# Optimization experiments

Measured on AMD Instinct MI355X. Metric: run time of the kernel, lower is better.

The kernel has to match this reference:

```python
import jax, jax.numpy as jnp
import numpy as np

EMBED = 512
HEADS = 8
HEAD_DIM = EMBED // HEADS
MLP_HIDDEN = EMBED * 4
EPS = 1e-5


def _layernorm(x, g, b):
    mu = jnp.mean(x, axis=-1, keepdims=True)
    var = jnp.var(x, axis=-1, keepdims=True)
    return (x - mu) * jax.lax.rsqrt(var + EPS) * g + b


def setup_inputs() -> dict:
    key = jax.random.key(0)
    ks = jax.random.split(key, 12)
    s = 0.02
    return {
        "x": jax.random.normal(ks[0], (4, 2048, EMBED), dtype=jnp.float32),
        "ln1_g": jnp.ones((EMBED,), jnp.float32),
        "ln1_b": jnp.zeros((EMBED,), jnp.float32),
        "w_qkv": jax.random.normal(ks[1], (EMBED, 3 * EMBED), jnp.float32) * s,
        "b_qkv": jnp.zeros((3 * EMBED,), jnp.float32),
        "w_proj": jax.random.normal(ks[2], (EMBED, EMBED), jnp.float32) * s,
        "b_proj": jnp.zeros((EMBED,), jnp.float32),
        "ln2_g": jnp.ones((EMBED,), jnp.float32),
        "ln2_b": jnp.zeros((EMBED,), jnp.float32),
        "w1": jax.random.normal(ks[3], (EMBED, MLP_HIDDEN), jnp.float32) * s,
        "b1": jnp.zeros((MLP_HIDDEN,), jnp.float32),
        "w2": jax.random.normal(ks[4], (MLP_HIDDEN, EMBED), jnp.float32) * s,
        "b2": jnp.zeros((EMBED,), jnp.float32),
    }


def reference(x, ln1_g, ln1_b, w_qkv, b_qkv, w_proj, b_proj, ln2_g, ln2_b, w1, b1, w2, b2):
    B, N, C = x.shape
    scale = HEAD_DIM ** -0.5
    h = _layernorm(x, ln1_g, ln1_b)
    qkv = h @ w_qkv + b_qkv                       # [B,N,3C]
    qkv = qkv.reshape(B, N, 3, HEADS, HEAD_DIM)
    q = qkv[:, :, 0].transpose(0, 2, 1, 3)        # [B,H,N,D]
    k = qkv[:, :, 1].transpose(0, 2, 1, 3)
    v = qkv[:, :, 2].transpose(0, 2, 1, 3)
    attn = jnp.einsum('bhnd,bhmd->bhnm', q, k) * scale
    attn = jax.nn.softmax(attn, axis=-1)
    h = jnp.einsum('bhnm,bhmd->bhnd', attn, v)    # [B,H,N,D]
    h = h.transpose(0, 2, 1, 3).reshape(B, N, C)
    h = h @ w_proj + b_proj
    x = x + h
    m = _layernorm(x, ln2_g, ln2_b)
    m = jax.nn.gelu(m @ w1 + b1, approximate=False) @ w2 + b2
    return x + m
```

## Files before the change

kernel.cpp:

```cpp
#include <hip/hip_runtime.h>
#include <hip/hip_bf16.h>

typedef unsigned short u16;
typedef unsigned int u32;
typedef __attribute__((ext_vector_type(8))) __bf16 bf16x8;
typedef __attribute__((ext_vector_type(4))) float f32x4;
typedef __attribute__((ext_vector_type(16))) float f32x16;

#define LOG2E 1.4426950408889634f

__device__ __forceinline__ u16 f2bf(float f) {
  union { __hip_bfloat16 h; u16 u; } cv;
  cv.h = __float2bfloat16(f);
  return cv.u;
}

__device__ __forceinline__ float bf2f(u16 u) {
  union { u32 u; float f; } cv;
  cv.u = ((u32)u) << 16;
  return cv.f;
}

__device__ __forceinline__ u32 pk2(float a, float b) {
  return (u32)f2bf(a) | ((u32)f2bf(b) << 16);
}

#define EXP2 __builtin_amdgcn_exp2f

__device__ __forceinline__ f32x4 mfma16(bf16x8 a, bf16x8 b, f32x4 c) {
  return __builtin_amdgcn_mfma_f32_16x16x32_bf16(a, b, c, 0, 0, 0);
}
__device__ __forceinline__ f32x16 mfma32(bf16x8 a, bf16x8 b, f32x16 c) {
  return __builtin_amdgcn_mfma_f32_32x32x16_bf16(a, b, c, 0, 0, 0);
}

__device__ __forceinline__ void gload16(const u16* g, u16* lds) {
  __builtin_amdgcn_global_load_lds(
      (const __attribute__((address_space(1))) u32*)g,
      (__attribute__((address_space(3))) u32*)lds, 16, 0, 0);
}

__global__ __launch_bounds__(256) void prep_kernel(
    const float* __restrict__ w_qkv, u16* __restrict__ wqkvT,
    const float* __restrict__ w_proj, u16* __restrict__ wprojT,
    const float* __restrict__ w1, u16* __restrict__ w1T,
    const float* __restrict__ w2, u16* __restrict__ w2T,
    const float* __restrict__ X, const float* __restrict__ gam,
    const float* __restrict__ bet, u16* __restrict__ Y) {
  __shared__ float T[64][65];
  const int bid = blockIdx.x;
  if (bid < 768) {
    const float* W; u16* WT; int K, N, base;
    if (bid < 192)      { W = w_qkv; WT = wqkvT; K = 512;  N = 1536; base = 0; }
    else if (bid < 256) { W = w_proj; WT = wprojT; K = 512; N = 512; base = 192; }
    else if (bid < 512) { W = w1;   WT = w1T;   K = 512;  N = 2048; base = 256; }
    else                { W = w2;   WT = w2T;   K = 2048; N = 512;  base = 512; }
    int b = bid - base;
    int ntx = N >> 6;
    int bx = b % ntx, by = b / ntx;
    int tx = threadIdx.x & 63, ty = threadIdx.x >> 6;
#pragma unroll
    for (int i = 0; i < 64; i += 4)
      T[ty + i][tx] = W[(size_t)(by * 64 + ty + i) * N + bx * 64 + tx];
    __syncthreads();
#pragma unroll
    for (int i = 0; i < 64; i += 4)
      WT[(size_t)(bx * 64 + ty + i) * K + by * 64 + tx] = f2bf(T[tx][ty + i]);
  } else {
    int wid = threadIdx.x >> 6, l = threadIdx.x & 63;
    int row = (bid - 768) * 4 + wid;
    const float4* xp = reinterpret_cast<const float4*>(X + (size_t)row * 512);
    float4 a = xp[l], c = xp[l + 64];
    float s  = a.x + a.y + a.z + a.w + c.x + c.y + c.z + c.w;
    float s2 = a.x*a.x + a.y*a.y + a.z*a.z + a.w*a.w
             + c.x*c.x + c.y*c.y + c.z*c.z + c.w*c.w;
#pragma unroll
    for (int m = 1; m < 64; m <<= 1) { s += __shfl_xor(s, m); s2 += __shfl_xor(s2, m); }
    float mu = s * (1.f / 512.f);
    float rs = rsqrtf(s2 * (1.f / 512.f) - mu * mu + 1e-5f);
    const float4* gp = reinterpret_cast<const float4*>(gam);
    const float4* bp = reinterpret_cast<const float4*>(bet);
    float4 g0 = gp[l], g1 = gp[l + 64], b0 = bp[l], b1 = bp[l + 64];
    ushort4 o;
    o.x = f2bf((a.x - mu) * rs * g0.x + b0.x);
    o.y = f2bf((a.y - mu) * rs * g0.y + b0.y);
    o.z = f2bf((a.z - mu) * rs * g0.z + b0.z);
    o.w = f2bf((a.w - mu) * rs * g0.w + b0.w);
    reinterpret_cast<ushort4*>(Y + (size_t)row * 512)[l] = o;
    o.x = f2bf((c.x - mu) * rs * g1.x + b1.x);
    o.y = f2bf((c.y - mu) * rs * g1.y + b1.y);
    o.z = f2bf((c.z - mu) * rs * g1.z + b1.z);
    o.w = f2bf((c.w - mu) * rs * g1.w + b1.w);
    reinterpret_cast<ushort4*>(Y + (size_t)row * 512)[l + 64] = o;
  }
}

__global__ __launch_bounds__(64) void ln_kernel(const float* __restrict__ X,
                                                const float* __restrict__ gam,
                                                const float* __restrict__ bet,
                                                u16* __restrict__ Y) {
  int row = blockIdx.x, l = threadIdx.x;
  const float4* xp = reinterpret_cast<const float4*>(X + (size_t)row * 512);
  float4 a = xp[l], c = xp[l + 64];
  float s  = a.x + a.y + a.z + a.w + c.x + c.y + c.z + c.w;
  float s2 = a.x*a.x + a.y*a.y + a.z*a.z + a.w*a.w
           + c.x*c.x + c.y*c.y + c.z*c.z + c.w*c.w;
#pragma unroll
  for (int m = 1; m < 64; m <<= 1) { s += __shfl_xor(s, m); s2 += __shfl_xor(s2, m); }
  float mu = s * (1.f / 512.f);
  float rs = rsqrtf(s2 * (1.f / 512.f) - mu * mu + 1e-5f);
  const float4* gp = reinterpret_cast<const float4*>(gam);
  const float4* bp = reinterpret_cast<const float4*>(bet);
  float4 g0 = gp[l], g1 = gp[l + 64], b0 = bp[l], b1 = bp[l + 64];
  ushort4 o;
  o.x = f2bf((a.x - mu) * rs * g0.x + b0.x);
  o.y = f2bf((a.y - mu) * rs * g0.y + b0.y);
  o.z = f2bf((a.z - mu) * rs * g0.z + b0.z);
  o.w = f2bf((a.w - mu) * rs * g0.w + b0.w);
  reinterpret_cast<ushort4*>(Y + (size_t)row * 512)[l] = o;
  o.x = f2bf((c.x - mu) * rs * g1.x + b1.x);
  o.y = f2bf((c.y - mu) * rs * g1.y + b1.y);
  o.z = f2bf((c.z - mu) * rs * g1.z + b1.z);
  o.w = f2bf((c.w - mu) * rs * g1.w + b1.w);
  reinterpret_cast<ushort4*>(Y + (size_t)row * 512)[l + 64] = o;
}

template <int EPI, int BM>
__global__ __launch_bounds__(256) void gemm_bt(
    const u16* __restrict__ A, const u16* __restrict__ BT,
    int M, int N, int K,
    const float* __restrict__ bias,
    const float* __restrict__ resid,
    float* __restrict__ outF,
    u16* __restrict__ outU,
    u16* __restrict__ Qo, u16* __restrict__ Ko, u16* __restrict__ VTo) {
  constexpr int MFR = BM / 32;
  constexpr int CA = BM / 64;
  __shared__ u16 As[2][BM * 32];
  __shared__ u16 Bs[2][128 * 32];
  const int tid = threadIdx.x;
  const int wid = tid >> 6, l = tid & 63;
  const int lg = l >> 4, ll = l & 15;
  const int nx = gridDim.x;
  const int id = blockIdx.y * nx + blockIdx.x;
  const int cpx = (nx * gridDim.y) >> 3;
  const int wg = (id & 7) * cpx + (id >> 3);
  const int m0 = (wg / nx) * BM, n0 = (wg % nx) * 128;
  const int wm = (wid >> 1) * (BM / 2), wn = (wid & 1) * 64;
  const f32x4 zf = {0.f, 0.f, 0.f, 0.f};
  f32x4 acc[MFR][4];
#pragma unroll
  for (int i = 0; i < MFR; i++)
#pragma unroll
    for (int j = 0; j < 4; j++) acc[i][j] = zf;

  int sArow[CA], sAcol[CA];
#pragma unroll
  for (int j = 0; j < CA; j++) {
    int p = (wid * CA + j) * 64 + l;
    sArow[j] = p >> 2;
    sAcol[j] = (p & 3) ^ ((sArow[j] >> 1) & 3);
  }
  int sBrow[2], sBcol[2];
#pragma unroll
  for (int j = 0; j < 2; j++) {
    int p = (wid * 2 + j) * 64 + l;
    sBrow[j] = p >> 2;
    sBcol[j] = (p & 3) ^ ((sBrow[j] >> 1) & 3);
  }
  int aoff[MFR], boff[4];
#pragma unroll
  for (int i = 0; i < MFR; i++) {
    int r = wm + i * 16 + ll;
    aoff[i] = (r * 4 + (lg ^ ((r >> 1) & 3))) * 8;
  }
#pragma unroll
  for (int j = 0; j < 4; j++) {
    int r = wn + j * 16 + ll;
    boff[j] = (r * 4 + (lg ^ ((r >> 1) & 3))) * 8;
  }

  auto stage = [&](int kt, int buf) {
#pragma unroll
    for (int j = 0; j < CA; j++)
      gload16(A + (size_t)(m0 + sArow[j]) * K + kt + sAcol[j] * 8,
              &As[buf][(wid * CA + j) * 512]);
#pragma unroll
    for (int j = 0; j < 2; j++)
      gload16(BT + (size_t)(n0 + sBrow[j]) * K + kt + sBcol[j] * 8,
              &Bs[buf][(wid * 2 + j) * 512]);
  };

  const int nt = K >> 5;
  stage(0, 0);
  for (int t = 0; t < nt; t++) {
    __syncthreads();
    if (t + 1 < nt) stage((t + 1) << 5, (t + 1) & 1);
    const u16* A_ = As[t & 1];
    const u16* B_ = Bs[t & 1];
    bf16x8 af[MFR], bfr[4];
#pragma unroll
    for (int i = 0; i < MFR; i++)
      af[i] = *reinterpret_cast<const bf16x8*>(A_ + aoff[i]);
#pragma unroll
    for (int j = 0; j < 4; j++)
      bfr[j] = *reinterpret_cast<const bf16x8*>(B_ + boff[j]);
#pragma unroll
    for (int i = 0; i < MFR; i++)
#pragma unroll
      for (int j = 0; j < 4; j++)
        acc[i][j] = mfma16(af[i], bfr[j], acc[i][j]);
  }

#pragma unroll
  for (int i = 0; i < MFR; i++) {
#pragma unroll
    for (int j = 0; j < 4; j++) {
      int col = n0 + wn + j * 16 + ll;
      float bcol2 = bias[col];
      int rbase = m0 + wm + i * 16 + lg * 4;
#pragma unroll
      for (int r = 0; r < 4; r++) {
        int row = rbase + r;
        float val = acc[i][j][r] + bcol2;
        if (EPI == 0) {
          int bi = row >> 11, nseq = row & 2047;
          int t = col >> 9, rem = col & 511;
          int hh = rem >> 6, dd = rem & 63;
          size_t hidx = ((size_t)((bi << 3) + hh) * 2048 + nseq) * 64 + dd;
          if (t == 0)      Qo[hidx] = f2bf(val * (0.125f * LOG2E));
          else if (t == 1) Ko[hidx] = f2bf(val);
          else VTo[((size_t)((bi << 3) + hh) * 64 + dd) * 2048 + nseq] = f2bf(val);
        } else if (EPI == 1) {
          size_t idx = (size_t)row * 512 + col;
          outF[idx] = val + resid[idx];
        } else if (EPI == 2) {
          float y = 0.7978845608f * (val + 0.044715f * val * val * val);
          float e = EXP2(2.0f * LOG2E * y);
          float t2 = 1.0f - 2.0f / (e + 1.0f);
          outU[(size_t)row * 2048 + col] = f2bf(0.5f * val * (1.0f + t2));
        } else {
          size_t idx = (size_t)row * 512 + col;
          outF[idx] = val + resid[idx];
        }
      }
    }
  }
}

__global__ __launch_bounds__(256)
__attribute__((amdgpu_waves_per_eu(4)))
void attn_kernel(const u16* __restrict__ Q,
                 const u16* __restrict__ Kt,
                 const u16* __restrict__ VT,
                 u16* __restrict__ Opart,
                 float* __restrict__ Stat) {
  __shared__ __align__(16) u16 Kbuf[2][64 * 64];
  __shared__ __align__(16) u16 Vbuf[2][64 * 64];
  const int tid = threadIdx.x;
  const int wid = tid >> 6, l = tid & 63;
  const int lq = l & 31, h = l >> 5;
  const int b = blockIdx.z, hd = blockIdx.y;
  const int qt = blockIdx.x >> 2, sp = blockIdx.x & 3;
  const int qbase = qt * 128 + wid * 32;
  const int kv0 = sp * 512;
  const size_t hoff = (size_t)(b * 8 + hd) * 2048 * 64;
  const u16* Qh = Q + hoff;
  const u16* Kh = Kt + hoff;
  const u16* Vh = VT + hoff;

  bf16x8 qf[4];
#pragma unroll
  for (int s = 0; s < 4; s++)
    qf[s] = *reinterpret_cast<const bf16x8*>(Qh + (size_t)(qbase + lq) * 64 + s * 16 + h * 8);

  int koff[4];
#pragma unroll
  for (int s = 0; s < 4; s++)
    koff[s] = (lq * 8 + ((s * 2 + h) ^ (lq & 7))) * 8;

  f32x16 oacc[2];
#pragma unroll
  for (int r = 0; r < 16; r++) { oacc[0][r] = 0.f; oacc[1][r] = 0.f; }
  float ps0 = 0.f, ps1 = 0.f;

  auto stage = [&](int kb, int buf) {
#pragma unroll
    for (int half = 0; half < 2; half++) {
      int g0 = half * 256 + wid * 64;
      int p = g0 + l;
      int row = p >> 3;
      int c = (p & 7) ^ (row & 7);
      gload16(Kh + (size_t)(kb + row) * 64 + c * 8, &Kbuf[buf][g0 * 8]);
      gload16(Vh + (size_t)row * 2048 + kb + c * 8, &Vbuf[buf][g0 * 8]);
    }
  };

  stage(kv0, 0);
  for (int i = 0; i < 8; i++) {
    __syncthreads();
    if (i < 7) stage(kv0 + (i + 1) * 64, (i + 1) & 1);
    const u16* Kc = Kbuf[i & 1];
    const u16* Vc = Vbuf[i & 1];

#pragma unroll
    for (int t = 0; t < 2; t++) {
      f32x16 st;
#pragma unroll
      for (int r = 0; r < 16; r++) st[r] = 0.f;
      __builtin_amdgcn_s_setprio(1);
      if (t == 0) {
#pragma unroll
        for (int s = 0; s < 4; s++)
          st = mfma32(*reinterpret_cast<const bf16x8*>(Kc + koff[s]), qf[s], st);
      } else {
#pragma unroll
        for (int s = 0; s < 4; s++)
          st = mfma32(*reinterpret_cast<const bf16x8*>(Kc + koff[s] + 2048), qf[s], st);
      }
      __builtin_amdgcn_s_setprio(0);

#pragma unroll
      for (int j = 0; j < 16; j += 4) {
        float p0 = EXP2(st[j + 0]);
        float p1 = EXP2(st[j + 1]);
        float p2 = EXP2(st[j + 2]);
        float p3 = EXP2(st[j + 3]);
        st[j + 0] = p0; st[j + 1] = p1; st[j + 2] = p2; st[j + 3] = p3;
        ps0 += p0 + p2; ps1 += p1 + p3;
      }

      u32 w0 = pk2(st[0], st[1]),   w1 = pk2(st[2], st[3]);
      u32 w2 = pk2(st[4], st[5]),   w3 = pk2(st[6], st[7]);
      u32 w4 = pk2(st[8], st[9]),   w5 = pk2(st[10], st[11]);
      u32 w6 = pk2(st[12], st[13]), w7 = pk2(st[14], st[15]);
      uint4 pa0, pa1;
#if __has_builtin(__builtin_amdgcn_permlane32_swap)
      auto r02 = __builtin_amdgcn_permlane32_swap(w0, w2, false, false);
      auto r13 = __builtin_amdgcn_permlane32_swap(w1, w3, false, false);
      auto r46 = __builtin_amdgcn_permlane32_swap(w4, w6, false, false);
      auto r57 = __builtin_amdgcn_permlane32_swap(w5, w7, false, false);
      pa0.x = (u32)r02[0]; pa0.y = (u32)r13[0]; pa0.z = (u32)r02[1]; pa0.w = (u32)r13[1];
      pa1.x = (u32)r46[0]; pa1.y = (u32)r57[0]; pa1.z = (u32)r46[1]; pa1.w = (u32)r57[1];
#else
      u32 ra, rb;
      ra = (u32)__shfl_xor((int)(h ? w0 : w2), 32);
      rb = (u32)__shfl_xor((int)(h ? w1 : w3), 32);
      pa0.x = h ? ra : w0; pa0.y = h ? rb : w1;
      pa0.z = h ? w0 : ra; pa0.w = h ? w1 : rb;
      ra = (u32)__shfl_xor((int)(h ? w4 : w6), 32);
      rb = (u32)__shfl_xor((int)(h ? w5 : w7), 32);
      pa1.x = h ? ra : w4; pa1.y = h ? rb : w5;
      pa1.z = h ? w4 : ra; pa1.w = h ? w5 : rb;
#endif
      union { uint4 u; bf16x8 v; } p0u, p1u;
      p0u.u = pa0; p1u.u = pa1;
      __builtin_amdgcn_s_setprio(1);
      if (t == 0) {
        oacc[0] = mfma32(p0u.v, *reinterpret_cast<const bf16x8*>(Vc + koff[0]), oacc[0]);
        oacc[0] = mfma32(p1u.v, *reinterpret_cast<const bf16x8*>(Vc + koff[1]), oacc[0]);
        oacc[1] = mfma32(p0u.v, *reinterpret_cast<const bf16x8*>(Vc + koff[0] + 2048), oacc[1]);
        oacc[1] = mfma32(p1u.v, *reinterpret_cast<const bf16x8*>(Vc + koff[1] + 2048), oacc[1]);
      } else {
        oacc[0] = mfma32(p0u.v, *reinterpret_cast<const bf16x8*>(Vc + koff[2]), oacc[0]);
        oacc[0] = mfma32(p1u.v, *reinterpret_cast<const bf16x8*>(Vc + koff[3]), oacc[0]);
        oacc[1] = mfma32(p0u.v, *reinterpret_cast<const bf16x8*>(Vc + koff[2] + 2048), oacc[1]);
        oacc[1] = mfma32(p1u.v, *reinterpret_cast<const bf16x8*>(Vc + koff[3] + 2048), oacc[1]);
      }
      __builtin_amdgcn_s_setprio(0);
    }
  }

  float lsum = ps0 + ps1;
  lsum += __shfl_xor(lsum, 32);

  u16* Op = Opart + (size_t)sp * 8192 * 512;
#pragma unroll
  for (int r = 0; r < 16; r++) {
    const int qr = (r & 3) + 8 * (r >> 2) + 4 * h;
    size_t row = (size_t)b * 2048 + qbase + qr;
#pragma unroll
    for (int dt = 0; dt < 2; dt++) {
      int col = hd * 64 + dt * 32 + lq;
      Op[row * 512 + col] = f2bf(oacc[dt][r]);
    }
  }
  if (h == 0)
    Stat[(size_t)sp * 32 * 2048 + (size_t)(b * 8 + hd) * 2048 + qbase + lq] = lsum;
}

__global__ __launch_bounds__(256) void attn_merge(const u16* __restrict__ Opart,
                                                  const float* __restrict__ Stat,
                                                  u16* __restrict__ O) {
  int gid = blockIdx.x * 256 + threadIdx.x;
  int row = gid >> 6;
  int c8 = (gid & 63) * 8;
  int hd = c8 >> 6;
  int bh = (row >> 11) * 8 + hd;
  int n = row & 2047;
  float L = 0.f;
  float acc[8];
#pragma unroll
  for (int j = 0; j < 8; j++) acc[j] = 0.f;
#pragma unroll
  for (int p = 0; p < 4; p++) {
    L += Stat[(size_t)p * 32 * 2048 + (size_t)bh * 2048 + n];
    const ushort4* pp = reinterpret_cast<const ushort4*>(
        Opart + (size_t)p * 8192 * 512 + (size_t)row * 512 + c8);
    ushort4 v0 = pp[0], v1 = pp[1];
    acc[0] += bf2f(v0.x); acc[1] += bf2f(v0.y);
    acc[2] += bf2f(v0.z); acc[3] += bf2f(v0.w);
    acc[4] += bf2f(v1.x); acc[5] += bf2f(v1.y);
    acc[6] += bf2f(v1.z); acc[7] += bf2f(v1.w);
  }
  float li = 1.0f / L;
  ushort4 o0, o1;
  o0.x = f2bf(acc[0] * li); o0.y = f2bf(acc[1] * li);
  o0.z = f2bf(acc[2] * li); o0.w = f2bf(acc[3] * li);
  o1.x = f2bf(acc[4] * li); o1.y = f2bf(acc[5] * li);
  o1.z = f2bf(acc[6] * li); o1.w = f2bf(acc[7] * li);
  ushort4* op = reinterpret_cast<ushort4*>(O + (size_t)row * 512 + c8);
  op[0] = o0;
  op[1] = o1;
}

extern "C" void kernel_launch(void* const* d_in, const int* in_sizes, int n_in,
                              void* d_out, int out_size, void* d_ws, size_t ws_size,
                              hipStream_t stream) {
  const float* x      = (const float*)d_in[0];
  const float* ln1_g  = (const float*)d_in[1];
  const float* ln1_b  = (const float*)d_in[2];
  const float* w_qkv  = (const float*)d_in[3];
  const float* b_qkv  = (const float*)d_in[4];
  const float* w_proj = (const float*)d_in[5];
  const float* b_proj = (const float*)d_in[6];
  const float* ln2_g  = (const float*)d_in[7];
  const float* ln2_b  = (const float*)d_in[8];
  const float* w1     = (const float*)d_in[9];
  const float* b1     = (const float*)d_in[10];
  const float* w2     = (const float*)d_in[11];
  const float* b2     = (const float*)d_in[12];
  float* out = (float*)d_out;

  const int M = 8192;
  char* w = (char*)d_ws;
  u16* wqkvT  = (u16*)w; w += (size_t)1536 * 512 * 2;
  u16* wprojT = (u16*)w; w += (size_t)512 * 512 * 2;
  u16* w1T    = (u16*)w; w += (size_t)2048 * 512 * 2;
  u16* w2T    = (u16*)w; w += (size_t)512 * 2048 * 2;
  u16* h1     = (u16*)w; w += (size_t)M * 512 * 2;
  u16* Qb     = (u16*)w; w += (size_t)M * 512 * 2;
  u16* Kb     = (u16*)w; w += (size_t)M * 512 * 2;
  u16* VTb    = (u16*)w; w += (size_t)M * 512 * 2;
  u16* attn   = (u16*)w; w += (size_t)M * 512 * 2;
  u16* h2     = (u16*)w; w += (size_t)M * 512 * 2;
  u16* mid    = (u16*)w; w += (size_t)M * 2048 * 2;
  float* Stat = (float*)w; w += (size_t)4 * 32 * 2048 * sizeof(float);
  u16* Opart = (u16*)mid;

  prep_kernel<<<2816, 256, 0, stream>>>(w_qkv, wqkvT, w_proj, wprojT,
                                        w1, w1T, w2, w2T,
                                        x, ln1_g, ln1_b, h1);

  gemm_bt<0, 128><<<dim3(1536 / 128, M / 128), 256, 0, stream>>>(
      h1, wqkvT, M, 1536, 512, b_qkv, nullptr, nullptr, nullptr, Qb, Kb, VTb);

  attn_kernel<<<dim3(64, 8, 4), 256, 0, stream>>>(Qb, Kb, VTb, Opart, Stat);
  attn_merge<<<M * 64 / 256, 256, 0, stream>>>(Opart, Stat, attn);

  gemm_bt<1, 64><<<dim3(512 / 128, M / 64), 256, 0, stream>>>(
      attn, wprojT, M, 512, 512, b_proj, x, out, nullptr, nullptr, nullptr, nullptr);

  ln_kernel<<<M, 64, 0, stream>>>(out, ln2_g, ln2_b, h2);

  gemm_bt<2, 128><<<dim3(2048 / 128, M / 128), 256, 0, stream>>>(
      h2, w1T, M, 2048, 512, b1, nullptr, nullptr, mid, nullptr, nullptr, nullptr);

  gemm_bt<3, 64><<<dim3(512 / 128, M / 64), 256, 0, stream>>>(
      mid, w2T, M, 512, 2048, b2, out, out, nullptr, nullptr, nullptr, nullptr);
}
```

Measured before the change: 181.1 us.

## Split GEMM tiles across more waves with 32-column warp tiles

Reworks the GEMM kernel so each wave computes a 32-column slice instead of 64. Large GEMMs now run 512-thread blocks with 8 waves on 128x128 tiles, and the projection and fc2 GEMMs switch to 64x64 tiles, doubling their grid. Each thread now issues a single 16-byte load per operand per K-step, and a waves-per-EU hint is added. The aim is more latency hiding and better CU fill, at the cost of less register-level fragment reuse per wave and more LDS reads per MFMA.

Result: faster. 177.1 us (-2.2%).

```diff
diff --git a/kernel.cpp b/kernel.cpp
--- a/kernel.cpp
+++ b/kernel.cpp
@@ -125,19 +125,19 @@
   reinterpret_cast<ushort4*>(Y + (size_t)row * 512)[l + 64] = o;
 }
 
-template <int EPI, int BM>
-__global__ __launch_bounds__(256) void gemm_bt(
-    const u16* __restrict__ A, const u16* __restrict__ BT,
-    int M, int N, int K,
-    const float* __restrict__ bias,
-    const float* __restrict__ resid,
-    float* __restrict__ outF,
-    u16* __restrict__ outU,
-    u16* __restrict__ Qo, u16* __restrict__ Ko, u16* __restrict__ VTo) {
-  constexpr int MFR = BM / 32;
-  constexpr int CA = BM / 64;
+template <int EPI, int BM, int BN, int WC>
+__global__ __launch_bounds__(128 * WC)
+__attribute__((amdgpu_waves_per_eu(4)))
+void gemm_bt(const u16* __restrict__ A, const u16* __restrict__ BT,
+             int M, int N, int K,
+             const float* __restrict__ bias,
+             const float* __restrict__ resid,
+             float* __restrict__ outF,
+             u16* __restrict__ outU,
+             u16* __restrict__ Qo, u16* __restrict__ Ko, u16* __restrict__ VTo) {
+  constexpr int FM = BM / 32;
   __shared__ u16 As[2][BM * 32];
-  __shared__ u16 Bs[2][128 * 32];
+  __shared__ u16 Bs[2][BN * 32];
   const int tid = threadIdx.x;
   const int wid = tid >> 6, l = tid & 63;
   const int lg = l >> 4, ll = l & 15;
@@ -145,77 +145,51 @@
   const int id = blockIdx.y * nx + blockIdx.x;
   const int cpx = (nx * gridDim.y) >> 3;
   const int wg = (id & 7) * cpx + (id >> 3);
-  const int m0 = (wg / nx) * BM, n0 = (wg % nx) * 128;
-  const int wm = (wid >> 1) * (BM / 2), wn = (wid & 1) * 64;
+  const int m0 = (wg / nx) * BM, n0 = (wg % nx) * BN;
+  const int wm = (wid / WC) * (BM / 2), wn = (wid % WC) * 32;
   const f32x4 zf = {0.f, 0.f, 0.f, 0.f};
-  f32x4 acc[MFR][4];
-#pragma unroll
-  for (int i = 0; i < MFR; i++)
-#pragma unroll
-    for (int j = 0; j < 4; j++) acc[i][j] = zf;
-
-  int sArow[CA], sAcol[CA];
-#pragma unroll
-  for (int j = 0; j < CA; j++) {
-    int p = (wid * CA + j) * 64 + l;
-    sArow[j] = p >> 2;
-    sAcol[j] = (p & 3) ^ ((sArow[j] >> 1) & 3);
-  }
-  int sBrow[2], sBcol[2];
-#pragma unroll
-  for (int j = 0; j < 2; j++) {
-    int p = (wid * 2 + j) * 64 + l;
-    sBrow[j] = p >> 2;
-    sBcol[j] = (p & 3) ^ ((sBrow[j] >> 1) & 3);
-  }
-  int aoff[MFR], boff[4];
-#pragma unroll
-  for (int i = 0; i < MFR; i++) {
-    int r = wm + i * 16 + ll;
-    aoff[i] = (r * 4 + (lg ^ ((r >> 1) & 3))) * 8;
-  }
-#pragma unroll
-  for (int j = 0; j < 4; j++) {
-    int r = wn + j * 16 + ll;
-    boff[j] = (r * 4 + (lg ^ ((r >> 1) & 3))) * 8;
-  }
-
-  auto stage = [&](int kt, int buf) {
-#pragma unroll
-    for (int j = 0; j < CA; j++)
-      gload16(A + (size_t)(m0 + sArow[j]) * K + kt + sAcol[j] * 8,
-              &As[buf][(wid * CA + j) * 512]);
-#pragma unroll
-    for (int j = 0; j < 2; j++)
-      gload16(BT + (size_t)(n0 + sBrow[j]) * K + kt + sBcol[j] * 8,
-              &Bs[buf][(wid * 2 + j) * 512]);
-  };
+  f32x4 acc[FM][2];
+#pragma unroll
+  for (int i = 0; i < FM; i++) { acc[i][0] = zf; acc[i][1] = zf; }
+
+  const int grow = tid >> 2;
+  const int gcol = (tid & 3) ^ ((grow >> 1) & 3);
+  const u16* Asrc = A + (size_t)(m0 + grow) * K + gcol * 8;
+  const u16* Bsrc = BT + (size_t)(n0 + grow) * K + gcol * 8;
+
+  const int r0a = wm + ll;
+  const int aoff0 = (r0a * 4 + (lg ^ ((r0a >> 1) & 3))) * 8;
+  const int r0b = wn + ll;
+  const int boff0 = (r0b * 4 + (lg ^ ((r0b >> 1) & 3))) * 8;
 
   const int nt = K >> 5;
-  stage(0, 0);
+  gload16(Asrc, &As[0][tid * 8]);
+  gload16(Bsrc, &Bs[0][tid * 8]);
   for (int t = 0; t < nt; t++) {
     __syncthreads();
-    if (t + 1 < nt) stage((t + 1) << 5, (t + 1) & 1);
+    if (t + 1 < nt) {
+      gload16(Asrc + ((t + 1) << 5), &As[(t + 1) & 1][tid * 8]);
+      gload16(Bsrc + ((t + 1) << 5), &Bs[(t + 1) & 1][tid * 8]);
+    }
     const u16* A_ = As[t & 1];
     const u16* B_ = Bs[t & 1];
-    bf16x8 af[MFR], bfr[4];
-#pragma unroll
-    for (int i = 0; i < MFR; i++)
-      af[i] = *reinterpret_cast<const bf16x8*>(A_ + aoff[i]);
-#pragma unroll
-    for (int j = 0; j < 4; j++)
-      bfr[j] = *reinterpret_cast<const bf16x8*>(B_ + boff[j]);
-#pragma unroll
-    for (int i = 0; i < MFR; i++)
-#pragma unroll
-      for (int j = 0; j < 4; j++)
-        acc[i][j] = mfma16(af[i], bfr[j], acc[i][j]);
-  }
-
-#pragma unroll
-  for (int i = 0; i < MFR; i++) {
-#pragma unroll
-    for (int j = 0; j < 4; j++) {
+    bf16x8 af[FM], bfr[2];
+#pragma unroll
+    for (int i = 0; i < FM; i++)
+      af[i] = *reinterpret_cast<const bf16x8*>(A_ + aoff0 + 512 * i);
+    bfr[0] = *reinterpret_cast<const bf16x8*>(B_ + boff0);
+    bfr[1] = *reinterpret_cast<const bf16x8*>(B_ + boff0 + 512);
+#pragma unroll
+    for (int i = 0; i < FM; i++) {
+      acc[i][0] = mfma16(af[i], bfr[0], acc[i][0]);
+      acc[i][1] = mfma16(af[i], bfr[1], acc[i][1]);
+    }
+  }
+
+#pragma unroll
+  for (int i = 0; i < FM; i++) {
+#pragma unroll
+    for (int j = 0; j < 2; j++) {
       int col = n0 + wn + j * 16 + ll;
       float bcol2 = bias[col];
       int rbase = m0 + wm + i * 16 + lg * 4;
@@ -462,20 +436,20 @@
                                         w1, w1T, w2, w2T,
                                         x, ln1_g, ln1_b, h1);
 
-  gemm_bt<0, 128><<<dim3(1536 / 128, M / 128), 256, 0, stream>>>(
+  gemm_bt<0, 128, 128, 4><<<dim3(1536 / 128, M / 128), 512, 0, stream>>>(
       h1, wqkvT, M, 1536, 512, b_qkv, nullptr, nullptr, nullptr, Qb, Kb, VTb);
 
   attn_kernel<<<dim3(64, 8, 4), 256, 0, stream>>>(Qb, Kb, VTb, Opart, Stat);
   attn_merge<<<M * 64 / 256, 256, 0, stream>>>(Opart, Stat, attn);
 
-  gemm_bt<1, 64><<<dim3(512 / 128, M / 64), 256, 0, stream>>>(
+  gemm_bt<1, 64, 64, 2><<<dim3(512 / 64, M / 64), 256, 0, stream>>>(
       attn, wprojT, M, 512, 512, b_proj, x, out, nullptr, nullptr, nullptr, nullptr);
 
   ln_kernel<<<M, 64, 0, stream>>>(out, ln2_g, ln2_b, h2);
 
-  gemm_bt<2, 128><<<dim3(2048 / 128, M / 128), 256, 0, stream>>>(
+  gemm_bt<2, 128, 128, 4><<<dim3(2048 / 128, M / 128), 512, 0, stream>>>(
       h2, w1T, M, 2048, 512, b1, nullptr, nullptr, mid, nullptr, nullptr, nullptr);
 
-  gemm_bt<3, 64><<<dim3(512 / 128, M / 64), 256, 0, stream>>>(
+  gemm_bt<3, 64, 64, 2><<<dim3(512 / 64, M / 64), 256, 0, stream>>>(
       mid, w2T, M, 512, 2048, b2, out, out, nullptr, nullptr, nullptr, nullptr);
 }
```
